# Performance work log

Hardware: AMD Instinct MI355X
Metric: run time of the kernel (lower is better)

Reference implementation:

```python
import jax, jax.numpy as jnp
import numpy as np
from jax import lax

K = 512          # num_embeddings
D = 64           # embedding_dim
BETA = 0.25      # commitment_cost


def _conv(x, w, b, stride, pad):
    y = lax.conv_general_dilated(x, w, (stride, stride), ((pad, pad), (pad, pad)),
                                 dimension_numbers=('NCHW', 'OIHW', 'NCHW'))
    return y + b[None, :, None, None]


def _convT(x, w, b, stride, k, pad):
    # transposed conv as lhs-dilated conv; w is OIHW with O=out_channels
    p = k - 1 - pad
    y = lax.conv_general_dilated(x, w, (1, 1), ((p, p), (p, p)),
                                 lhs_dilation=(stride, stride),
                                 dimension_numbers=('NCHW', 'OIHW', 'NCHW'))
    return y + b[None, :, None, None]


def setup_inputs() -> dict:
    key = jax.random.key(0)
    ks = jax.random.split(key, 16)
    s = 0.05
    inp = {
        'x':   jax.random.uniform(ks[0], (16, 3, 256, 256), jnp.float32),
        'w1':  jax.random.normal(ks[1], (128, 3, 4, 4), jnp.float32) * s,
        'b1':  jnp.zeros((128,), jnp.float32),
        'w2':  jax.random.normal(ks[2], (256, 128, 4, 4), jnp.float32) * s,
        'b2':  jnp.zeros((256,), jnp.float32),
        'w3':  jax.random.normal(ks[3], (D, 256, 3, 3), jnp.float32) * s,
        'b3':  jnp.zeros((D,), jnp.float32),
        'emb': jax.random.uniform(ks[4], (K, D), jnp.float32, -1.0 / K, 1.0 / K),
        'wt1': jax.random.normal(ks[5], (256, D, 4, 4), jnp.float32) * s,
        'bt1': jnp.zeros((256,), jnp.float32),
        'wt2': jax.random.normal(ks[6], (128, 256, 4, 4), jnp.float32) * s,
        'bt2': jnp.zeros((128,), jnp.float32),
        'w4':  jax.random.normal(ks[7], (3, 128, 3, 3), jnp.float32) * s,
        'b4':  jnp.zeros((3,), jnp.float32),
    }
    return inp


def reference(x, w1, b1, w2, b2, w3, b3, emb, wt1, bt1, wt2, bt2, w4, b4):
    # ---- encoder ----
    h = jax.nn.relu(_conv(x, w1, b1, 2, 1))    # [B,128,128,128]
    h = jax.nn.relu(_conv(h, w2, b2, 2, 1))    # [B,256,64,64]
    z = _conv(h, w3, b3, 1, 1)                 # [B,64,64,64]

    # ---- vector quantizer (faithful raw-memory reshape, as in source) ----
    flat_z = z.reshape(-1, D)                                 # [N,D]
    dists = (jnp.sum(flat_z ** 2, axis=1, keepdims=True)
             + jnp.sum(emb ** 2, axis=1)
             - 2.0 * flat_z @ emb.T)                          # [N,K]
    idx = jnp.argmin(dists, axis=1)                           # [N]
    quantized = emb[idx].reshape(z.shape)                     # gather == onehot @ emb

    e_latent = jnp.mean((lax.stop_gradient(quantized) - z) ** 2)
    q_latent = jnp.mean((quantized - lax.stop_gradient(z)) ** 2)
    vq_loss = q_latent + BETA * e_latent

    z_q = z + lax.stop_gradient(quantized - z)                # straight-through

    n = flat_z.shape[0]
    avg_probs = jnp.zeros((K,), jnp.float32).at[idx].add(1.0) / n
    perplexity = jnp.exp(-jnp.sum(avg_probs * jnp.log(avg_probs + 1e-10)))

    # ---- decoder (computed in the original forward; its output is unused) ----
    d = jax.nn.relu(_convT(z_q, wt1, bt1, 2, 4, 1))           # [B,256,128,128]
    d = jax.nn.relu(_convT(d, wt2, bt2, 2, 4, 1))             # [B,128,256,256]
    _x_recon = jax.nn.sigmoid(_conv(d, w4, b4, 1, 1))         # [B,3,256,256]

    return (z_q, vq_loss, perplexity)
```

## Files before the change

### kernel.cpp

```cpp
#include <hip/hip_runtime.h>
#include <math.h>

typedef __attribute__((ext_vector_type(8))) short bf16x8;
typedef __attribute__((ext_vector_type(4))) float f32x4;
typedef __attribute__((ext_vector_type(4))) unsigned u32x4;
typedef __attribute__((ext_vector_type(2))) unsigned u32x2;

#define H1P_OFF  0ull
#define H2P_OFF  35143680ull
#define WQ2H_OFF 53526528ull
#define WQ2L_OFF 53788672ull
#define WQ3H_OFF 54050816ull
#define WQ3L_OFF 54149120ull
#define EQ_OFF   54247424ull
#define EN_OFF   54280192ull
#define HIST_OFF 54280704ull
#define SSEP_OFF 54284800ull
#define WQ1H_OFF 54285824ull
#define WQ1L_OFF 54289920ull

__device__ inline unsigned short f2bf(float f) {
  unsigned u = __builtin_bit_cast(unsigned, f);
  return (unsigned short)((u + 0x7fffu + ((u >> 16) & 1u)) >> 16);
}
__device__ inline float bf2f(unsigned short h) {
  return __builtin_bit_cast(float, (unsigned)h << 16);
}
__device__ inline unsigned packsplit(float v) {
  unsigned short h = f2bf(v);
  unsigned short l = f2bf(v - bf2f(h));
  return (unsigned)h | ((unsigned)l << 16);
}
#define SEL_HI 0x05040100u
#define SEL_LO 0x07060302u
__device__ inline bf16x8 mkfrag(const u32x4 p, const u32x4 q, unsigned sel) {
  u32x4 r;
  r[0] = __builtin_amdgcn_perm(p[1], p[0], sel);
  r[1] = __builtin_amdgcn_perm(p[3], p[2], sel);
  r[2] = __builtin_amdgcn_perm(q[1], q[0], sel);
  r[3] = __builtin_amdgcn_perm(q[3], q[2], sel);
  return __builtin_bit_cast(bf16x8, r);
}

__global__ void pack_wq1_k(const float* __restrict__ w, unsigned short* __restrict__ wh) {
  int i = blockIdx.x * 256 + threadIdx.x;
  if (i >= 8192) return;
  int j = i & 7, l = (i >> 3) & 63, fg = (i >> 9) & 7, ks = i >> 12;
  int row = fg * 16 + (l & 15);
  int k = ks * 32 + (l >> 4) * 8 + j;
  int ci = k >> 4, r = k & 15, kh = r >> 2, kw = r & 3;
  wh[i] = (ci < 3) ? f2bf(w[((row * 3 + ci) * 4 + kh) * 4 + kw]) : (unsigned short)0;
}
__global__ void pack_wq2_k(const float* __restrict__ w, unsigned short* __restrict__ wh) {
  int i = blockIdx.x * 256 + threadIdx.x;
  if (i >= 524288) return;
  int j = i & 7, l = (i >> 3) & 63, fg = (i >> 9) & 15, ks = i >> 13;
  int row = fg * 16 + (l & 15);
  int k = ks * 32 + (l >> 4) * 8 + j;
  wh[i] = f2bf(w[row * 2048 + k]);
}
__global__ void pack_wq3_k(const float* __restrict__ w, unsigned short* __restrict__ wh) {
  int i = blockIdx.x * 256 + threadIdx.x;
  if (i >= 196608) return;
  int j = i & 7, l = (i >> 3) & 63, fg = (i >> 9) & 3, ks = i >> 11;
  int row = fg * 16 + (l & 15);
  int k = ks * 32 + (l >> 4) * 8 + j;
  int ci = k / 12, rb = k - ci * 12, kh = rb >> 2, kw = rb & 3;
  wh[i] = (kw < 3) ? f2bf(w[((row * 256 + ci) * 3 + kh) * 3 + kw]) : (unsigned short)0;
}
__global__ void pack_eq_k(const float* __restrict__ emb, unsigned* __restrict__ eq,
                          float* __restrict__ enorm) {
  int i = blockIdx.x * 256 + threadIdx.x;
  if (i < 32768) {
    int e = i & 3, l = (i >> 2) & 63, j = (i >> 8) & 1, fg = (i >> 9) & 31, ks = i >> 14;
    int row = fg * 16 + (l & 15);
    int d = ks * 32 + (l >> 4) * 8 + j * 4 + e;
    eq[i] = packsplit(emb[row * 64 + d]);
  }
  if (i < 512) {
    float s = 0.f;
#pragma unroll
    for (int d = 0; d < 64; ++d) { float e = emb[i * 64 + d]; s += e * e; }
    enorm[i] = s;
  }
}

__global__ void pack_x1_k(const float* __restrict__ x, unsigned* __restrict__ xp) {
  int i = blockIdx.x * 256 + threadIdx.x;
  if (i >= 16 * 4 * 258 * 260) return;
  int b = i / 268320, r = i - b * 268320;
  int ci = r / 67080, r2 = r - ci * 67080;
  int iy = r2 / 260, ix = r2 - iy * 260;
  unsigned v = 0u;
  if (ci < 3 && iy >= 1 && iy <= 256 && ix >= 1 && ix <= 256)
    v = packsplit(x[((b * 3 + ci) * 256 + (iy - 1)) * 256 + (ix - 1)]);
  xp[i] = v;
}

__global__ void halo_k(unsigned* __restrict__ h1p, unsigned* __restrict__ h2p) {
  int i = blockIdx.x * 256 + threadIdx.x;
  if (i < 2048 * 520) {
    int p = i / 520, c = i - p * 520; int r, cc;
    if (c < 132)      { r = 0;   cc = c; }
    else if (c < 264) { r = 129; cc = c - 132; }
    else if (c < 392) { r = c - 264 + 1; cc = 0; }
    else              { r = c - 392 + 1; cc = 129; }
    h1p[(size_t)p * 130 * 132 + r * 132 + cc] = 0u;
  } else {
    int j = i - 2048 * 520;
    if (j >= 4096 * 328) return;
    int p = j / 328, c = j - p * 328; int r, cc;
    if (c < 68)       { r = 0;  cc = c; }
    else if (c < 136) { r = 65; cc = c - 68; }
    else { int c2 = c - 136; int which = c2 >> 6; r = 1 + (c2 & 63);
           cc = (which == 0) ? 0 : (which == 1 ? 65 : 66); }
    h2p[(size_t)p * 66 * 68 + r * 68 + cc] = 0u;
  }
}

template <int IC, int KHW, int OC, int IHP, int IWP, int S, int NWX, int NWC,
          int YB, bool WIDE, int OSR, int OSP, int OPAD, bool SPLIT_OUT>
__global__ __launch_bounds__(256, 2) void convmm_k(const unsigned* __restrict__ inp,
                                                   const unsigned short* __restrict__ wqh,
                                                   const float* __restrict__ bias,
                                                   unsigned* __restrict__ outp,
                                                   float* __restrict__ outf) {
  constexpr int K = IC * KHW;
  constexpr int KSTEPS = K / 32;
  constexpr int FGTOT = OC / 16;
  constexpr int NFRAG = OC / NWC / 16;
  constexpr int MR = 64 * NWX;
  constexpr int CELLS = MR / 32;
  constexpr int GPLANE = MR * 16;
  constexpr int HBYTES = MR * 64;
  constexpr int ABYTES = MR * 128;
  constexpr int LOG2NWX = (NWX == 2) ? 1 : 0;

  __shared__ char smem[2 * ABYTES];

  const int tid = threadIdx.x, l = tid & 63, wv = tid >> 6;
  const int orig = (blockIdx.x & 7) * ((int)gridDim.x >> 3) + (blockIdx.x >> 3);
  const int bb = orig >> YB;
  const int y0 = orig & ((1 << YB) - 1);
  const int rsel = l & 15, gp = l >> 4;
  const int mbase = (wv & (NWX - 1)) * 64;
  const int fgbase = (wv >> LOG2NWX) * NFRAG;
  const int nbase = fgbase * 16;

  const int arow = tid & (MR - 1);
  int qs[CELLS];
  const unsigned* abase[CELLS];
#pragma unroll
  for (int c = 0; c < CELLS; ++c) {
    if constexpr (NWX == 1) qs[c] = (tid >> 6) * 2 + c;
    else                    qs[c] = (tid >> 7) * 4 + c;
    if constexpr (KHW == 16) {
      int ci0 = qs[c] >> 2, kh = qs[c] & 3;
      abase[c] = inp + (((size_t)bb * IC + ci0) * IHP + (S * y0 + kh)) * IWP + S * arow;
    }
  }

  f32x4 acc[NFRAG][4];
#pragma unroll
  for (int nf = 0; nf < NFRAG; ++nf)
#pragma unroll
    for (int xf = 0; xf < 4; ++xf) acc[nf][xf] = (f32x4){0.f, 0.f, 0.f, 0.f};

  unsigned avA[CELLS][4], avB[CELLS][4];
  bf16x8 brA[NFRAG], brB[NFRAG];

  auto loadA = [&](int ks, unsigned (&av)[CELLS][4]) {
#pragma unroll
    for (int c = 0; c < CELLS; ++c) {
      if constexpr (KHW == 16) {
        const unsigned* p = abase[c];
        av[c][0] = p[0]; av[c][1] = p[1]; av[c][2] = p[2]; av[c][3] = p[3];
        abase[c] += (size_t)2 * IHP * IWP;
      } else {
        int k = ks * 32 + qs[c] * 4;
        int ci = (k * 5462) >> 16;
        int rb = k - ci * 12;
        int kh = rb >> 2;
        int yl = arow >> 6, x = arow & 63;
        const unsigned* p = inp + (((size_t)bb * IC + ci) * IHP + (y0 * 2 + yl + kh)) * IWP + x;
        av[c][0] = p[0]; av[c][1] = p[1]; av[c][2] = p[2]; av[c][3] = p[3];
      }
    }
  };
  auto writeA = [&](int buf, unsigned (&av)[CELLS][4]) {
    char* base = smem + buf * ABYTES;
#pragma unroll
    for (int cp = 0; cp < CELLS / 2; ++cp) {
      int q0 = qs[2 * cp];
      int off = (q0 >> 1) * GPLANE + (arow << 4);
      u32x4 h, lo;
      h[0]  = __builtin_amdgcn_perm(av[2 * cp][1],     av[2 * cp][0],     SEL_HI);
      h[1]  = __builtin_amdgcn_perm(av[2 * cp][3],     av[2 * cp][2],     SEL_HI);
      h[2]  = __builtin_amdgcn_perm(av[2 * cp + 1][1], av[2 * cp + 1][0], SEL_HI);
      h[3]  = __builtin_amdgcn_perm(av[2 * cp + 1][3], av[2 * cp + 1][2], SEL_HI);
      lo[0] = __builtin_amdgcn_perm(av[2 * cp][1],     av[2 * cp][0],     SEL_LO);
      lo[1] = __builtin_amdgcn_perm(av[2 * cp][3],     av[2 * cp][2],     SEL_LO);
      lo[2] = __builtin_amdgcn_perm(av[2 * cp + 1][1], av[2 * cp + 1][0], SEL_LO);
      lo[3] = __builtin_amdgcn_perm(av[2 * cp + 1][3], av[2 * cp + 1][2], SEL_LO);
      *(u32x4*)(base + off) = h;
      *(u32x4*)(base + HBYTES + off) = lo;
    }
  };
  auto loadB = [&](int ks, bf16x8 (&bh)[NFRAG]) {
#pragma unroll
    for (int nf = 0; nf < NFRAG; ++nf) {
      size_t idx = (((size_t)(ks * FGTOT + fgbase + nf) * 64) + l) * 8;
      bh[nf] = *(const bf16x8*)(wqh + idx);
    }
  };
  auto step = [&](int ks, bf16x8 (&ch)[NFRAG], bf16x8 (&nh)[NFRAG],
                  unsigned (&avW)[CELLS][4], unsigned (&avL)[CELLS][4]) {
    const bool hasW = (ks + 1 < KSTEPS);
    const bool hasL = (ks + 2 < KSTEPS);
    if (hasW) loadB(ks + 1, nh);
    if (hasL) loadA(ks + 2, avL);
    const char* bA = smem + (ks & 1) * ABYTES;
    bf16x8 ah[4], al[4];
#pragma unroll
    for (int xf = 0; xf < 4; ++xf) {
      int row = mbase + xf * 16 + rsel;
      ah[xf] = *(const bf16x8*)(bA + gp * GPLANE + (row << 4));
      al[xf] = *(const bf16x8*)(bA + HBYTES + gp * GPLANE + (row << 4));
    }
#pragma unroll
    for (int nf = 0; nf < NFRAG; ++nf) {
#pragma unroll
      for (int xf = 0; xf < 4; ++xf) {
        acc[nf][xf] = __builtin_amdgcn_mfma_f32_16x16x32_bf16(ch[nf], ah[xf], acc[nf][xf], 0, 0, 0);
        acc[nf][xf] = __builtin_amdgcn_mfma_f32_16x16x32_bf16(ch[nf], al[xf], acc[nf][xf], 0, 0, 0);
      }
    }
    if (hasW) writeA((ks & 1) ^ 1, avW);
    __syncthreads();
  };

  loadB(0, brA);
  loadA(0, avA);
  writeA(0, avA);
  if (KSTEPS > 1) loadA(1, avB);
  __syncthreads();

#pragma unroll 1
  for (int ks = 0; ks < KSTEPS; ks += 2) {
    step(ks,     brA, brB, avB, avA);
    step(ks + 1, brB, brA, avA, avB);
  }

#pragma unroll
  for (int nf = 0; nf < NFRAG; ++nf) {
    int n0 = nbase + nf * 16 + (l >> 4) * 4;
#pragma unroll
    for (int xf = 0; xf < 4; ++xf) {
      int m = mbase + xf * 16 + rsel;
      int xo, yout;
      if constexpr (WIDE) { xo = m; yout = y0; }
      else { xo = m & 63; yout = y0 * NWX + (m >> 6); }
#pragma unroll
      for (int r = 0; r < 4; ++r) {
        float v = acc[nf][xf][r] + bias[n0 + r];
        if constexpr (SPLIT_OUT) {
          if (v < 0.f) v = 0.f;
          outp[((size_t)bb * OC + n0 + r) * OSP + (size_t)(yout + OPAD) * OSR + (xo + OPAD)] =
              packsplit(v);
        } else {
          outf[((size_t)bb * OC + n0 + r) * OSP + (size_t)yout * OSR + xo] = v;
        }
      }
    }
  }
}

__global__ __launch_bounds__(256, 2) void vqmm_k(float* __restrict__ zq,
                                                 const float* __restrict__ emb,
                                                 const unsigned* __restrict__ eq,
                                                 const float* __restrict__ enorm,
                                                 unsigned* __restrict__ hist,
                                                 float* __restrict__ ssep) {
  const int tid = threadIdx.x, l = tid & 63, wv = tid >> 6;
  float* zsrc = zq + (size_t)blockIdx.x * 4096;

  __shared__ float zf[64][64];
  __shared__ unsigned zp[4096];
  __shared__ float candd[4][64];
  __shared__ int   candi[4][64];
  __shared__ int   idxf[64];
  __shared__ unsigned hcnt[512];
  __shared__ float wsse[4];

  for (int i = tid; i < 512; i += 256) hcnt[i] = 0;

#pragma unroll
  for (int p = 0; p < 4; ++p) {
    int idx = p * 256 + tid;
    float4 v = *(const float4*)(zsrc + (size_t)idx * 4);
    int n = idx >> 4, d0 = (idx & 15) * 4;
    zf[n][d0 + 0] = v.x; zf[n][d0 + 1] = v.y;
    zf[n][d0 + 2] = v.z; zf[n][d0 + 3] = v.w;
  }
  __syncthreads();
#pragma unroll
  for (int p = 0; p < 16; ++p) {
    int idx = p * 256 + tid;
    int n = idx >> 6, d = idx & 63;
    zp[(n << 6) + ((((d >> 2) ^ (n & 15)) << 2) | (d & 3))] = packsplit(zf[n][d]);
  }
  __syncthreads();

  f32x4 acc[8][4];
#pragma unroll
  for (int nf = 0; nf < 8; ++nf)
#pragma unroll
    for (int xf = 0; xf < 4; ++xf) acc[nf][xf] = (f32x4){0.f, 0.f, 0.f, 0.f};

  const int rsel = l & 15;
#pragma unroll
  for (int ks = 0; ks < 2; ++ks) {
    bf16x8 ah[4], al[4];
    const int gk = ks * 8 + (l >> 4) * 2;
#pragma unroll
    for (int xf = 0; xf < 4; ++xf) {
      int n = xf * 16 + rsel;
      u32x4 p0 = *(const u32x4*)((const char*)zp + (n << 8) + ((gk ^ (n & 15)) << 4));
      u32x4 p1 = *(const u32x4*)((const char*)zp + (n << 8) + (((gk + 1) ^ (n & 15)) << 4));
      ah[xf] = mkfrag(p0, p1, SEL_HI);
      al[xf] = mkfrag(p0, p1, SEL_LO);
    }
#pragma unroll
    for (int nf = 0; nf < 8; ++nf) {
      int fg = wv * 8 + nf;
      u32x4 b0 = *(const u32x4*)(eq + (((size_t)((ks * 32 + fg) * 2 + 0)) << 8) + (l << 2));
      u32x4 b1 = *(const u32x4*)(eq + (((size_t)((ks * 32 + fg) * 2 + 1)) << 8) + (l << 2));
      bf16x8 wh = mkfrag(b0, b1, SEL_HI);
      bf16x8 wl = mkfrag(b0, b1, SEL_LO);
#pragma unroll
      for (int xf = 0; xf < 4; ++xf) {
        acc[nf][xf] = __builtin_amdgcn_mfma_f32_16x16x32_bf16(wh, ah[xf], acc[nf][xf], 0, 0, 0);
        acc[nf][xf] = __builtin_amdgcn_mfma_f32_16x16x32_bf16(wh, al[xf], acc[nf][xf], 0, 0, 0);
        acc[nf][xf] = __builtin_amdgcn_mfma_f32_16x16x32_bf16(wl, ah[xf], acc[nf][xf], 0, 0, 0);
      }
    }
  }

  float en[8][4];
#pragma unroll
  for (int nf = 0; nf < 8; ++nf)
#pragma unroll
    for (int r = 0; r < 4; ++r)
      en[nf][r] = enorm[wv * 128 + nf * 16 + (l >> 4) * 4 + r];

#pragma unroll
  for (int xf = 0; xf < 4; ++xf) {
    float best = 1e30f; int bidx = 0;
#pragma unroll
    for (int nf = 0; nf < 8; ++nf)
#pragma unroll
      for (int r = 0; r < 4; ++r) {
        int k = wv * 128 + nf * 16 + (l >> 4) * 4 + r;
        float dist = en[nf][r] - 2.f * acc[nf][xf][r];
        if (dist < best || (dist == best && k < bidx)) { best = dist; bidx = k; }
      }
#pragma unroll
    for (int off = 16; off <= 32; off <<= 1) {
      float ob = __shfl_xor(best, off, 64);
      int oi = __shfl_xor(bidx, off, 64);
      if (ob < best || (ob == best && oi < bidx)) { best = ob; bidx = oi; }
    }
    if (l < 16) { candd[wv][xf * 16 + l] = best; candi[wv][xf * 16 + l] = bidx; }
  }
  __syncthreads();
  if (tid < 64) {
    float best = candd[0][tid]; int bidx = candi[0][tid];
#pragma unroll
    for (int w = 1; w < 4; ++w) {
      float ob = candd[w][tid]; int oi = candi[w][tid];
      if (ob < best || (ob == best && oi < bidx)) { best = ob; bidx = oi; }
    }
    idxf[tid] = bidx;
    atomicAdd(&hcnt[bidx], 1u);
  }
  __syncthreads();

  float sse = 0.f;
#pragma unroll
  for (int p = 0; p < 16; ++p) {
    int idx = p * 256 + tid;
    int n = idx >> 6, d = idx & 63;
    float q = emb[idxf[n] * 64 + d];
    float z = zf[n][d];
    float df = q - z;
    sse += df * df;
    zsrc[idx] = q;
  }
#pragma unroll
  for (int off = 32; off > 0; off >>= 1) sse += __shfl_down(sse, off, 64);
  if (l == 0) wsse[wv] = sse;

  unsigned* hr = hist + ((blockIdx.x & 7) << 9);
  __syncthreads();
  for (int i = tid; i < 512; i += 256)
    if (hcnt[i]) atomicAdd(&hr[i], hcnt[i]);
  if (tid == 0) ssep[blockIdx.x] = wsse[0] + wsse[1] + wsse[2] + wsse[3];
}

__global__ void fin_k(const unsigned* __restrict__ hist,
                      const float* __restrict__ ssep,
                      float* __restrict__ out) {
  __shared__ float red[512];
  __shared__ float sred[512];
  int t = threadIdx.x;
  sred[t] = ssep[t] + ssep[t + 512];
  unsigned c = 0;
#pragma unroll
  for (int r = 0; r < 8; ++r) c += hist[(r << 9) + t];
  float p = (float)c * (1.f / 65536.f);
  red[t] = p * logf(p + 1e-10f);
  __syncthreads();
  for (int s = 256; s > 0; s >>= 1) {
    if (t < s) { red[t] += red[t + s]; sred[t] += sred[t + s]; }
    __syncthreads();
  }
  if (t == 0) {
    out[4194304] = 1.25f * sred[0] * (1.f / 4194304.f);
    out[4194305] = expf(-red[0]);
  }
}

extern "C" void kernel_launch(void* const* d_in, const int* in_sizes, int n_in,
                              void* d_out, int out_size, void* d_ws, size_t ws_size,
                              hipStream_t stream) {
  const float* x   = (const float*)d_in[0];
  const float* w1  = (const float*)d_in[1];
  const float* b1  = (const float*)d_in[2];
  const float* w2  = (const float*)d_in[3];
  const float* b2  = (const float*)d_in[4];
  const float* w3  = (const float*)d_in[5];
  const float* b3  = (const float*)d_in[6];
  const float* emb = (const float*)d_in[7];

  float* out = (float*)d_out;
  unsigned* wsu = (unsigned*)d_ws;
  unsigned* h1p = wsu + H1P_OFF;
  unsigned* h2p = wsu + H2P_OFF;
  unsigned* x1p = wsu + H2P_OFF;
  unsigned short* wq1h = (unsigned short*)(wsu + WQ1H_OFF);
  unsigned short* wq2h = (unsigned short*)(wsu + WQ2H_OFF);
  unsigned short* wq3h = (unsigned short*)(wsu + WQ3H_OFF);
  unsigned* eqp = wsu + EQ_OFF;
  float* enorm = (float*)(wsu + EN_OFF);
  unsigned* hist = wsu + HIST_OFF;
  float* ssep = (float*)(wsu + SSEP_OFF);

  hipMemsetAsync(wsu + HIST_OFF, 0, 4096 * sizeof(unsigned), stream);

  pack_wq1_k<<<dim3(32),   dim3(256), 0, stream>>>(w1, wq1h);
  pack_wq2_k<<<dim3(2048), dim3(256), 0, stream>>>(w2, wq2h);
  pack_wq3_k<<<dim3(768),  dim3(256), 0, stream>>>(w3, wq3h);
  pack_eq_k<<<dim3(128),   dim3(256), 0, stream>>>(emb, eqp, enorm);
  pack_x1_k<<<dim3(16770), dim3(256), 0, stream>>>(x, x1p);

  convmm_k<4, 16, 128, 258, 260, 2, 2, 2, 7, true, 132, 17160, 1, true>
      <<<dim3(2048), dim3(256), 0, stream>>>(x1p, wq1h, b1, h1p, nullptr);
  halo_k<<<dim3(9408), dim3(256), 0, stream>>>(h1p, h2p);
  convmm_k<128, 16, 256, 130, 132, 2, 1, 4, 6, false, 68, 4488, 1, true>
      <<<dim3(1024), dim3(256), 0, stream>>>(h1p, wq2h, b2, h2p, nullptr);
  convmm_k<256, 12, 64, 66, 68, 1, 2, 2, 5, false, 64, 4096, 0, false>
      <<<dim3(512), dim3(256), 0, stream>>>(h2p, wq3h, b3, nullptr, out);

  vqmm_k<<<dim3(1024), dim3(256), 0, stream>>>(out, emb, eqp, enorm, hist, ssep);
  fin_k<<<dim3(1), dim3(512), 0, stream>>>(hist, ssep, out);
}
```

Baseline: 296.6 us.

## Process two K-steps per barrier in conv GEMM kernels for conv2 and conv3

Adds a template depth parameter so each pipeline stage stages D K-chunks of A in shared memory and loads D sets of B fragments. The main loop then runs half as many iterations, with half as many __syncthreads, for conv2 and conv3. In exchange it doubles LDS usage and register pressure, which may lower occupancy or cause spills under launch_bounds(256,2).

```diff
diff --git a/kernel.cpp b/kernel.cpp
--- a/kernel.cpp
+++ b/kernel.cpp
@@ -119,22 +119,23 @@
 }
 
 template <int IC, int KHW, int OC, int IHP, int IWP, int S, int NWX, int NWC,
-          int YB, bool WIDE, int OSR, int OSP, int OPAD, bool SPLIT_OUT>
+          int YB, bool WIDE, int OSR, int OSP, int OPAD, bool SPLIT_OUT, int D>
 __global__ __launch_bounds__(256, 2) void convmm_k(const unsigned* __restrict__ inp,
                                                    const unsigned short* __restrict__ wqh,
                                                    const float* __restrict__ bias,
                                                    unsigned* __restrict__ outp,
                                                    float* __restrict__ outf) {
   constexpr int K = IC * KHW;
-  constexpr int KSTEPS = K / 32;
+  constexpr int KSUPER = K / (32 * D);
   constexpr int FGTOT = OC / 16;
   constexpr int NFRAG = OC / NWC / 16;
   constexpr int MR = 64 * NWX;
-  constexpr int CELLS = MR / 32;
+  constexpr int CELLS = (MR / 32) * D;
   constexpr int GPLANE = MR * 16;
-  constexpr int HBYTES = MR * 64;
-  constexpr int ABYTES = MR * 128;
+  constexpr int HBYTES = MR * 64 * D;
+  constexpr int ABYTES = MR * 128 * D;
   constexpr int LOG2NWX = (NWX == 2) ? 1 : 0;
+  constexpr int LOG2MR = (NWX == 2) ? 7 : 6;
 
   __shared__ char smem[2 * ABYTES];
 
@@ -152,8 +153,7 @@
   const unsigned* abase[CELLS];
 #pragma unroll
   for (int c = 0; c < CELLS; ++c) {
-    if constexpr (NWX == 1) qs[c] = (tid >> 6) * 2 + c;
-    else                    qs[c] = (tid >> 7) * 4 + c;
+    qs[c] = (tid >> LOG2MR) * CELLS + c;
     if constexpr (KHW == 16) {
       int ci0 = qs[c] >> 2, kh = qs[c] & 3;
       abase[c] = inp + (((size_t)bb * IC + ci0) * IHP + (S * y0 + kh)) * IWP + S * arow;
@@ -167,7 +167,7 @@
     for (int xf = 0; xf < 4; ++xf) acc[nf][xf] = (f32x4){0.f, 0.f, 0.f, 0.f};
 
   unsigned avA[CELLS][4], avB[CELLS][4];
-  bf16x8 brA[NFRAG], brB[NFRAG];
+  bf16x8 brA[D][NFRAG], brB[D][NFRAG];
 
   auto loadA = [&](int ks, unsigned (&av)[CELLS][4]) {
 #pragma unroll
@@ -175,9 +175,9 @@
       if constexpr (KHW == 16) {
         const unsigned* p = abase[c];
         av[c][0] = p[0]; av[c][1] = p[1]; av[c][2] = p[2]; av[c][3] = p[3];
-        abase[c] += (size_t)2 * IHP * IWP;
+        abase[c] += (size_t)(2 * D) * IHP * IWP;
       } else {
-        int k = ks * 32 + qs[c] * 4;
+        int k = ks * (32 * D) + qs[c] * 4;
         int ci = (k * 5462) >> 16;
         int rb = k - ci * 12;
         int kh = rb >> 2;
@@ -206,33 +206,38 @@
       *(u32x4*)(base + HBYTES + off) = lo;
     }
   };
-  auto loadB = [&](int ks, bf16x8 (&bh)[NFRAG]) {
-#pragma unroll
-    for (int nf = 0; nf < NFRAG; ++nf) {
-      size_t idx = (((size_t)(ks * FGTOT + fgbase + nf) * 64) + l) * 8;
-      bh[nf] = *(const bf16x8*)(wqh + idx);
-    }
+  auto loadB = [&](int ks, bf16x8 (&bh)[D][NFRAG]) {
+#pragma unroll
+    for (int s = 0; s < D; ++s)
+#pragma unroll
+      for (int nf = 0; nf < NFRAG; ++nf) {
+        size_t idx = (((size_t)((ks * D + s) * FGTOT + fgbase + nf) * 64) + l) * 8;
+        bh[s][nf] = *(const bf16x8*)(wqh + idx);
+      }
   };
-  auto step = [&](int ks, bf16x8 (&ch)[NFRAG], bf16x8 (&nh)[NFRAG],
+  auto step = [&](int ks, bf16x8 (&ch)[D][NFRAG], bf16x8 (&nh)[D][NFRAG],
                   unsigned (&avW)[CELLS][4], unsigned (&avL)[CELLS][4]) {
-    const bool hasW = (ks + 1 < KSTEPS);
-    const bool hasL = (ks + 2 < KSTEPS);
+    const bool hasW = (ks + 1 < KSUPER);
+    const bool hasL = (ks + 2 < KSUPER);
     if (hasW) loadB(ks + 1, nh);
     if (hasL) loadA(ks + 2, avL);
     const char* bA = smem + (ks & 1) * ABYTES;
-    bf16x8 ah[4], al[4];
-#pragma unroll
-    for (int xf = 0; xf < 4; ++xf) {
-      int row = mbase + xf * 16 + rsel;
-      ah[xf] = *(const bf16x8*)(bA + gp * GPLANE + (row << 4));
-      al[xf] = *(const bf16x8*)(bA + HBYTES + gp * GPLANE + (row << 4));
-    }
-#pragma unroll
-    for (int nf = 0; nf < NFRAG; ++nf) {
+#pragma unroll
+    for (int s = 0; s < D; ++s) {
+      bf16x8 ah[4], al[4];
 #pragma unroll
       for (int xf = 0; xf < 4; ++xf) {
-        acc[nf][xf] = __builtin_amdgcn_mfma_f32_16x16x32_bf16(ch[nf], ah[xf], acc[nf][xf], 0, 0, 0);
-        acc[nf][xf] = __builtin_amdgcn_mfma_f32_16x16x32_bf16(ch[nf], al[xf], acc[nf][xf], 0, 0, 0);
+        int row = mbase + xf * 16 + rsel;
+        ah[xf] = *(const bf16x8*)(bA + (s * 4 + gp) * GPLANE + (row << 4));
+        al[xf] = *(const bf16x8*)(bA + HBYTES + (s * 4 + gp) * GPLANE + (row << 4));
+      }
+#pragma unroll
+      for (int nf = 0; nf < NFRAG; ++nf) {
+#pragma unroll
+        for (int xf = 0; xf < 4; ++xf) {
+          acc[nf][xf] = __builtin_amdgcn_mfma_f32_16x16x32_bf16(ch[s][nf], ah[xf], acc[nf][xf], 0, 0, 0);
+          acc[nf][xf] = __builtin_amdgcn_mfma_f32_16x16x32_bf16(ch[s][nf], al[xf], acc[nf][xf], 0, 0, 0);
+        }
       }
     }
     if (hasW) writeA((ks & 1) ^ 1, avW);
@@ -242,11 +247,11 @@
   loadB(0, brA);
   loadA(0, avA);
   writeA(0, avA);
-  if (KSTEPS > 1) loadA(1, avB);
+  if (KSUPER > 1) loadA(1, avB);
   __syncthreads();
 
 #pragma unroll 1
-  for (int ks = 0; ks < KSTEPS; ks += 2) {
+  for (int ks = 0; ks < KSUPER; ks += 2) {
     step(ks,     brA, brB, avB, avA);
     step(ks + 1, brB, brA, avA, avB);
   }
@@ -463,12 +468,12 @@
   pack_eq_k<<<dim3(128),   dim3(256), 0, stream>>>(emb, eqp, enorm);
   pack_x1_k<<<dim3(16770), dim3(256), 0, stream>>>(x, x1p);
 
-  convmm_k<4, 16, 128, 258, 260, 2, 2, 2, 7, true, 132, 17160, 1, true>
+  convmm_k<4, 16, 128, 258, 260, 2, 2, 2, 7, true, 132, 17160, 1, true, 1>
       <<<dim3(2048), dim3(256), 0, stream>>>(x1p, wq1h, b1, h1p, nullptr);
   halo_k<<<dim3(9408), dim3(256), 0, stream>>>(h1p, h2p);
-  convmm_k<128, 16, 256, 130, 132, 2, 1, 4, 6, false, 68, 4488, 1, true>
+  convmm_k<128, 16, 256, 130, 132, 2, 1, 4, 6, false, 68, 4488, 1, true, 2>
       <<<dim3(1024), dim3(256), 0, stream>>>(h1p, wq2h, b2, h2p, nullptr);
-  convmm_k<256, 12, 64, 66, 68, 1, 2, 2, 5, false, 64, 4096, 0, false>
+  convmm_k<256, 12, 64, 66, 68, 1, 2, 2, 5, false, 64, 4096, 0, false, 2>
       <<<dim3(512), dim3(256), 0, stream>>>(h2p, wq3h, b3, nullptr, out);
 
   vqmm_k<<<dim3(1024), dim3(256), 0, stream>>>(out, emb, eqp, enorm, hist, ssep);
```

Result: no change. 292.7 us (-1.3%).
